# Kernel tuning notes

Measured on AMD Instinct MI355X. Metric: run time of the kernel, lower is better.

## Reference

```python
import jax, jax.numpy as jnp
import numpy as np

B, LQ, LD, H, C = 128, 32, 512, 768, 128


def setup_inputs() -> dict:
    key = jax.random.key(0)
    ks = jax.random.split(key, 8)
    return {
        "query_hidden": jax.random.normal(ks[0], (B, LQ, H), dtype=jnp.float32),
        "doc_hidden": jax.random.normal(ks[1], (B, LD, H), dtype=jnp.float32),
        "query_mask": jax.random.randint(ks[2], (B, LQ), 0, 2, dtype=jnp.int32),
        "doc_mask": jax.random.randint(ks[3], (B, LD), 0, 2, dtype=jnp.int32),
        "W_comp": jax.random.normal(ks[4], (H, C), dtype=jnp.float32) * (1.0 / np.sqrt(H)),
        "b_comp": jax.random.normal(ks[5], (C,), dtype=jnp.float32) * 0.02,
        "w_stop": jax.random.normal(ks[6], (C, 1), dtype=jnp.float32) * (1.0 / np.sqrt(C)),
        "b_stop": jnp.ones((1,), dtype=jnp.float32),  # nn.init.constant_(bias, 1)
        "score_merger": jnp.zeros((1,), dtype=jnp.float32),
    }


def reference(query_hidden, doc_hidden, query_mask, doc_mask,
              W_comp, b_comp, w_stop, b_stop, score_merger):
    qm = query_mask.astype(bool)  # [B, LQ]
    dm = doc_mask.astype(bool)    # [B, LD]

    # encode_shared: CLS vec is the UNcompressed hidden state at position 0
    q_cls = query_hidden[:, 0, :]  # [B, H]
    d_cls = doc_hidden[:, 0, :]    # [B, H]

    # compressor (Linear H->C)
    q_vecs = jnp.einsum('blh,hc->blc', query_hidden, W_comp) + b_comp  # [B, LQ, C]
    d_tok = jnp.einsum('blh,hc->blc', doc_hidden, W_comp) + b_comp     # [B, LD, C]

    # encode_query: zero masked query tokens
    q_vecs = q_vecs * qm[..., None]

    # encode_doc: stopword reducer (relu of Linear C->1), then importance + mask
    importance = jax.nn.relu(jnp.einsum('blc,co->blo', d_tok, w_stop) + b_stop)  # [B, LD, 1]
    d_vecs = d_tok * importance * dm[..., None]

    # CLS score: dot product of (uncompressed) CLS vectors
    cls_score = jnp.sum(q_cls * d_cls, axis=-1)  # [B]

    # term score: MaxSim over doc tokens, masked sum over query tokens
    scores = jnp.einsum('bqc,bkc->bqk', q_vecs, d_vecs)      # [B, LQ, LD]
    scores = jnp.where(dm[:, None, :], scores, -1000.0)
    term = jnp.max(scores, axis=-1)                          # [B, LQ]
    term_score = jnp.sum(jnp.where(qm, term, 0.0), axis=-1)  # [B]

    w = jax.nn.sigmoid(score_merger[0])
    cls_score = cls_score * w
    term_score = term_score * (1.0 - w)
    score = cls_score + term_score
    return (score, cls_score, term_score)
```

## Files before the change

kernel.cpp:

```cpp
#include <hip/hip_runtime.h>
#include <hip/hip_bf16.h>

#define Bb 128
#define LQ 32
#define LD 512
#define Hh 768
#define Cc 128

typedef short bf16x8 __attribute__((ext_vector_type(8)));
typedef float f32x4 __attribute__((ext_vector_type(4)));

__device__ __forceinline__ short f2bf(float f) {
  union { float f; unsigned u; } v;
  v.f = f;
  unsigned u = v.u + (0x7FFFu + ((v.u >> 16) & 1u));
  return (short)(u >> 16);
}

__global__ __launch_bounds__(256) void k_wt(const float* __restrict__ W,
                                            short* __restrict__ Wt) {
  int idx = blockIdx.x * 256 + threadIdx.x;
  int h = idx >> 7;
  int c = idx & 127;
  Wt[c * Hh + h] = f2bf(W[idx]);
}

template <int IS_DOC>
__global__ __launch_bounds__(256) void k_proj(
    const float* __restrict__ X, const short* __restrict__ Wt,
    const float* __restrict__ bcomp, const int* __restrict__ mask,
    const float* __restrict__ wstop, const float* __restrict__ bstop,
    float* __restrict__ Y) {
  const int tid = threadIdx.x;
  const int wave = tid >> 6;
  const int lane = tid & 63;
  const int quad = lane >> 4;
  const int lm = lane & 15;
  const long row0 = (long)blockIdx.x * 128 + wave * 32;

  const float* pa0 = X + (row0 + lm) * Hh + quad * 8;
  const float* pa1 = pa0 + 16 * Hh;
  const short* pbb = Wt + lm * Hh + quad * 8;

  f32x4 acc[2][8];
#pragma unroll
  for (int i = 0; i < 2; ++i)
#pragma unroll
    for (int j = 0; j < 8; ++j) acc[i][j] = (f32x4){0.f, 0.f, 0.f, 0.f};

  for (int kk = 0; kk < Hh; kk += 32) {
    float4 a0l = *(const float4*)(pa0 + kk);
    float4 a0h = *(const float4*)(pa0 + kk + 4);
    float4 a1l = *(const float4*)(pa1 + kk);
    float4 a1h = *(const float4*)(pa1 + kk + 4);
    bf16x8 fb[8];
#pragma unroll
    for (int j = 0; j < 8; ++j)
      fb[j] = *(const bf16x8*)(pbb + j * 16 * Hh + kk);
    bf16x8 fa0, fa1;
    fa0[0] = f2bf(a0l.x); fa0[1] = f2bf(a0l.y);
    fa0[2] = f2bf(a0l.z); fa0[3] = f2bf(a0l.w);
    fa0[4] = f2bf(a0h.x); fa0[5] = f2bf(a0h.y);
    fa0[6] = f2bf(a0h.z); fa0[7] = f2bf(a0h.w);
    fa1[0] = f2bf(a1l.x); fa1[1] = f2bf(a1l.y);
    fa1[2] = f2bf(a1l.z); fa1[3] = f2bf(a1l.w);
    fa1[4] = f2bf(a1h.x); fa1[5] = f2bf(a1h.y);
    fa1[6] = f2bf(a1h.z); fa1[7] = f2bf(a1h.w);
#pragma unroll
    for (int j = 0; j < 8; ++j) {
      acc[0][j] = __builtin_amdgcn_mfma_f32_16x16x32_bf16(fa0, fb[j], acc[0][j], 0, 0, 0);
      acc[1][j] = __builtin_amdgcn_mfma_f32_16x16x32_bf16(fa1, fb[j], acc[1][j], 0, 0, 0);
    }
  }

  float bc[8], ws[8];
#pragma unroll
  for (int j = 0; j < 8; ++j) bc[j] = bcomp[j * 16 + lm];
  if (IS_DOC) {
#pragma unroll
    for (int j = 0; j < 8; ++j) ws[j] = wstop[j * 16 + lm];
  }
  const float bs = IS_DOC ? bstop[0] : 0.f;

#pragma unroll
  for (int i = 0; i < 2; ++i) {
#pragma unroll
    for (int r = 0; r < 4; ++r) {
      const long row = row0 + i * 16 + quad * 4 + r;
      float v[8];
#pragma unroll
      for (int j = 0; j < 8; ++j) v[j] = acc[i][j][r] + bc[j];
      float scale;
      if (IS_DOC) {
        float p = 0.f;
#pragma unroll
        for (int j = 0; j < 8; ++j) p += v[j] * ws[j];
        p += __shfl_xor(p, 1);
        p += __shfl_xor(p, 2);
        p += __shfl_xor(p, 4);
        p += __shfl_xor(p, 8);
        float imp = fmaxf(p + bs, 0.f);
        scale = imp * (float)mask[row];
      } else {
        scale = (float)mask[row];
      }
      float* yr = Y + row * Cc;
#pragma unroll
      for (int j = 0; j < 8; ++j) yr[j * 16 + lm] = v[j] * scale;
    }
  }
}

__global__ __launch_bounds__(256) void k_scores(
    const float* __restrict__ Qv, const float* __restrict__ Dv,
    const int* __restrict__ dmask, float* __restrict__ partial) {
  const int chunk = blockIdx.x;
  const int b = blockIdx.y;
  const int tid = threadIdx.x;
  __shared__ float lq[LQ][Cc + 4];
  __shared__ float ldv[64][Cc + 4];
  __shared__ float pm[LQ][16];
  __shared__ int dmsk[64];

  {
    const float4* src = (const float4*)(Qv + (size_t)b * LQ * Cc);
    for (int i = tid; i < LQ * Cc / 4; i += 256) {
      float4 v = src[i];
      int q = i >> 5;
      int c = (i & 31) << 2;
      *(float4*)&lq[q][c] = v;
    }
  }
  const int k0 = chunk * 64;
  {
    const float4* src = (const float4*)(Dv + ((size_t)b * LD + k0) * Cc);
    for (int i = tid; i < 64 * Cc / 4; i += 256) {
      float4 v = src[i];
      int k = i >> 5;
      int c = (i & 31) << 2;
      *(float4*)&ldv[k][c] = v;
    }
  }
  if (tid < 64) dmsk[tid] = dmask[(size_t)b * LD + k0 + tid];
  __syncthreads();

  const int qt = tid & 15;
  const int kt = tid >> 4;
  const int kbase = kt * 4;
  float a[2][4];
#pragma unroll
  for (int qi = 0; qi < 2; ++qi)
#pragma unroll
    for (int ki = 0; ki < 4; ++ki) a[qi][ki] = 0.f;

  for (int c = 0; c < Cc; c += 4) {
    float4 q0 = *(float4*)&lq[qt][c];
    float4 q1 = *(float4*)&lq[qt + 16][c];
    float4 d0 = *(float4*)&ldv[kbase + 0][c];
    float4 d1 = *(float4*)&ldv[kbase + 1][c];
    float4 d2 = *(float4*)&ldv[kbase + 2][c];
    float4 d3 = *(float4*)&ldv[kbase + 3][c];
    a[0][0] += q0.x * d0.x + q0.y * d0.y + q0.z * d0.z + q0.w * d0.w;
    a[0][1] += q0.x * d1.x + q0.y * d1.y + q0.z * d1.z + q0.w * d1.w;
    a[0][2] += q0.x * d2.x + q0.y * d2.y + q0.z * d2.z + q0.w * d2.w;
    a[0][3] += q0.x * d3.x + q0.y * d3.y + q0.z * d3.z + q0.w * d3.w;
    a[1][0] += q1.x * d0.x + q1.y * d0.y + q1.z * d0.z + q1.w * d0.w;
    a[1][1] += q1.x * d1.x + q1.y * d1.y + q1.z * d1.z + q1.w * d1.w;
    a[1][2] += q1.x * d2.x + q1.y * d2.y + q1.z * d2.z + q1.w * d2.w;
    a[1][3] += q1.x * d3.x + q1.y * d3.y + q1.z * d3.z + q1.w * d3.w;
  }
  float m0 = -1000.f, m1 = -1000.f;
#pragma unroll
  for (int ki = 0; ki < 4; ++ki) {
    if (dmsk[kbase + ki]) {
      m0 = fmaxf(m0, a[0][ki]);
      m1 = fmaxf(m1, a[1][ki]);
    }
  }
  pm[qt][kt] = m0;
  pm[qt + 16][kt] = m1;
  __syncthreads();
  if (tid < LQ) {
    float mx = pm[tid][0];
#pragma unroll
    for (int t = 1; t < 16; ++t) mx = fmaxf(mx, pm[tid][t]);
    partial[((size_t)b * LQ + tid) * 8 + chunk] = mx;
  }
}

__global__ __launch_bounds__(256) void k_final(
    const float* __restrict__ qh, const float* __restrict__ dh,
    const int* __restrict__ qmask, const float* __restrict__ partial,
    const float* __restrict__ merger, float* __restrict__ out) {
  const int b = blockIdx.x;
  const int tid = threadIdx.x;
  __shared__ float red[256];
  __shared__ float clss;
  const float* qc = qh + (size_t)b * LQ * Hh;
  const float* dc = dh + (size_t)b * LD * Hh;
  float s = 0.f;
  for (int h = tid; h < Hh; h += 256) s += qc[h] * dc[h];
  red[tid] = s;
  __syncthreads();
  for (int off = 128; off > 0; off >>= 1) {
    if (tid < off) red[tid] += red[tid + off];
    __syncthreads();
  }
  if (tid == 0) clss = red[0];
  __syncthreads();
  float t = 0.f;
  if (tid < LQ) {
    const float* pp = partial + ((size_t)b * LQ + tid) * 8;
    float mx = pp[0];
#pragma unroll
    for (int c = 1; c < 8; ++c) mx = fmaxf(mx, pp[c]);
    if (qmask[b * LQ + tid]) t = mx;
  }
  red[tid] = t;
  __syncthreads();
  for (int off = 128; off > 0; off >>= 1) {
    if (tid < off) red[tid] += red[tid + off];
    __syncthreads();
  }
  if (tid == 0) {
    float w = 1.f / (1.f + expf(-merger[0]));
    float cs = clss * w;
    float ts = red[0] * (1.f - w);
    out[b] = cs + ts;
    out[Bb + b] = cs;
    out[2 * Bb + b] = ts;
  }
}

extern "C" void kernel_launch(void* const* d_in, const int* in_sizes, int n_in,
                              void* d_out, int out_size, void* d_ws, size_t ws_size,
                              hipStream_t stream) {
  const float* qh  = (const float*)d_in[0];
  const float* dh  = (const float*)d_in[1];
  const int*   qm  = (const int*)d_in[2];
  const int*   dm  = (const int*)d_in[3];
  const float* W   = (const float*)d_in[4];
  const float* bc  = (const float*)d_in[5];
  const float* wst = (const float*)d_in[6];
  const float* bst = (const float*)d_in[7];
  const float* mrg = (const float*)d_in[8];
  float* out = (float*)d_out;

  char* ws = (char*)d_ws;
  short* Wt  = (short*)ws;
  float* qv  = (float*)(ws + 196608);
  float* dv  = (float*)(ws + 196608 + 2097152);
  float* prt = (float*)(ws + 196608 + 2097152 + 33554432);

  k_wt<<<(Hh * Cc) / 256, 256, 0, stream>>>(W, Wt);
  k_proj<0><<<(Bb * LQ) / 128, 256, 0, stream>>>(qh, Wt, bc, qm, nullptr, nullptr, qv);
  k_proj<1><<<(Bb * LD) / 128, 256, 0, stream>>>(dh, Wt, bc, dm, wst, bst, dv);
  k_scores<<<dim3(8, Bb), 256, 0, stream>>>(qv, dv, dm, prt);
  k_final<<<Bb, 256, 0, stream>>>(qh, dh, qm, prt, mrg, out);
}
```

Measured before the change: 398.3 us.

## Merge query and doc projections into one launch with smaller tiles and prefetch

Replaces the two templated projection kernels with a single launch that covers both doc and query rows, dispatching on block index. Each wave now handles 16 rows instead of 32, doubling the block count to improve occupancy and CU coverage. The A operand is software-prefetched one 64-wide K step ahead to hide global load latency. The cost is that each W tile is reused across fewer rows, so more W traffic per row, and the prefetch adds registers and a redundant wraparound load on the last iteration.

```diff
diff --git a/kernel.cpp b/kernel.cpp
--- a/kernel.cpp
+++ b/kernel.cpp
@@ -7,6 +7,9 @@
 #define Hh 768
 #define Cc 128
 
+#define QBLOCKS ((Bb * LQ) / 64)
+#define DBLOCKS ((Bb * LD) / 64)
+
 typedef short bf16x8 __attribute__((ext_vector_type(8)));
 typedef float f32x4 __attribute__((ext_vector_type(4)));
 
@@ -15,6 +18,11 @@
   v.f = f;
   unsigned u = v.u + (0x7FFFu + ((v.u >> 16) & 1u));
   return (short)(u >> 16);
+}
+
+__device__ __forceinline__ void pack8(bf16x8& d, const float4& lo, const float4& hi) {
+  d[0] = f2bf(lo.x); d[1] = f2bf(lo.y); d[2] = f2bf(lo.z); d[3] = f2bf(lo.w);
+  d[4] = f2bf(hi.x); d[5] = f2bf(hi.y); d[6] = f2bf(hi.z); d[7] = f2bf(hi.w);
 }
 
 __global__ __launch_bounds__(256) void k_wt(const float* __restrict__ W,
@@ -25,89 +33,100 @@
   Wt[c * Hh + h] = f2bf(W[idx]);
 }
 
-template <int IS_DOC>
-__global__ __launch_bounds__(256) void k_proj(
-    const float* __restrict__ X, const short* __restrict__ Wt,
-    const float* __restrict__ bcomp, const int* __restrict__ mask,
+__global__ __launch_bounds__(256) void k_proj_all(
+    const float* __restrict__ qh, const float* __restrict__ dh,
+    const short* __restrict__ Wt, const float* __restrict__ bcomp,
+    const int* __restrict__ qmask, const int* __restrict__ dmask,
     const float* __restrict__ wstop, const float* __restrict__ bstop,
-    float* __restrict__ Y) {
+    float* __restrict__ qv, float* __restrict__ dv) {
   const int tid = threadIdx.x;
   const int wave = tid >> 6;
   const int lane = tid & 63;
   const int quad = lane >> 4;
   const int lm = lane & 15;
-  const long row0 = (long)blockIdx.x * 128 + wave * 32;
-
-  const float* pa0 = X + (row0 + lm) * Hh + quad * 8;
-  const float* pa1 = pa0 + 16 * Hh;
-  const short* pbb = Wt + lm * Hh + quad * 8;
-
-  f32x4 acc[2][8];
-#pragma unroll
-  for (int i = 0; i < 2; ++i)
-#pragma unroll
-    for (int j = 0; j < 8; ++j) acc[i][j] = (f32x4){0.f, 0.f, 0.f, 0.f};
-
-  for (int kk = 0; kk < Hh; kk += 32) {
-    float4 a0l = *(const float4*)(pa0 + kk);
-    float4 a0h = *(const float4*)(pa0 + kk + 4);
-    float4 a1l = *(const float4*)(pa1 + kk);
-    float4 a1h = *(const float4*)(pa1 + kk + 4);
-    bf16x8 fb[8];
-#pragma unroll
-    for (int j = 0; j < 8; ++j)
-      fb[j] = *(const bf16x8*)(pbb + j * 16 * Hh + kk);
-    bf16x8 fa0, fa1;
-    fa0[0] = f2bf(a0l.x); fa0[1] = f2bf(a0l.y);
-    fa0[2] = f2bf(a0l.z); fa0[3] = f2bf(a0l.w);
-    fa0[4] = f2bf(a0h.x); fa0[5] = f2bf(a0h.y);
-    fa0[6] = f2bf(a0h.z); fa0[7] = f2bf(a0h.w);
-    fa1[0] = f2bf(a1l.x); fa1[1] = f2bf(a1l.y);
-    fa1[2] = f2bf(a1l.z); fa1[3] = f2bf(a1l.w);
-    fa1[4] = f2bf(a1h.x); fa1[5] = f2bf(a1h.y);
-    fa1[6] = f2bf(a1h.z); fa1[7] = f2bf(a1h.w);
+
+  const int blk = blockIdx.x;
+  const bool is_doc = blk < DBLOCKS;
+  const float* X;
+  float* Y;
+  const int* mask;
+  long row0;
+  if (is_doc) {
+    X = dh; Y = dv; mask = dmask;
+    row0 = (long)blk * 64 + wave * 16;
+  } else {
+    X = qh; Y = qv; mask = qmask;
+    row0 = (long)(blk - DBLOCKS) * 64 + wave * 16;
+  }
+
+  const float* pa = X + (row0 + lm) * (long)Hh + quad * 8;
+  const short* pb = Wt + lm * Hh + quad * 8;
+
+  f32x4 acc[8];
+#pragma unroll
+  for (int j = 0; j < 8; ++j) acc[j] = (f32x4){0.f, 0.f, 0.f, 0.f};
+
+  float4 c0 = *(const float4*)(pa);
+  float4 c1 = *(const float4*)(pa + 4);
+  float4 c2 = *(const float4*)(pa + 32);
+  float4 c3 = *(const float4*)(pa + 36);
+
+  for (int kk = 0; kk < Hh; kk += 64) {
+    int kn = kk + 64;
+    if (kn >= Hh) kn = 0;
+    float4 n0 = *(const float4*)(pa + kn);
+    float4 n1 = *(const float4*)(pa + kn + 4);
+    float4 n2 = *(const float4*)(pa + kn + 32);
+    float4 n3 = *(const float4*)(pa + kn + 36);
+
+    bf16x8 fa;
+    pack8(fa, c0, c1);
 #pragma unroll
     for (int j = 0; j < 8; ++j) {
-      acc[0][j] = __builtin_amdgcn_mfma_f32_16x16x32_bf16(fa0, fb[j], acc[0][j], 0, 0, 0);
-      acc[1][j] = __builtin_amdgcn_mfma_f32_16x16x32_bf16(fa1, fb[j], acc[1][j], 0, 0, 0);
-    }
-  }
-
-  float bc[8], ws[8];
+      bf16x8 fb = *(const bf16x8*)(pb + j * 16 * Hh + kk);
+      acc[j] = __builtin_amdgcn_mfma_f32_16x16x32_bf16(fa, fb, acc[j], 0, 0, 0);
+    }
+    pack8(fa, c2, c3);
+#pragma unroll
+    for (int j = 0; j < 8; ++j) {
+      bf16x8 fb = *(const bf16x8*)(pb + j * 16 * Hh + kk + 32);
+      acc[j] = __builtin_amdgcn_mfma_f32_16x16x32_bf16(fa, fb, acc[j], 0, 0, 0);
+    }
+    c0 = n0; c1 = n1; c2 = n2; c3 = n3;
+  }
+
+  float bc[8], wsv[8];
 #pragma unroll
   for (int j = 0; j < 8; ++j) bc[j] = bcomp[j * 16 + lm];
-  if (IS_DOC) {
-#pragma unroll
-    for (int j = 0; j < 8; ++j) ws[j] = wstop[j * 16 + lm];
-  }
-  const float bs = IS_DOC ? bstop[0] : 0.f;
-
-#pragma unroll
-  for (int i = 0; i < 2; ++i) {
-#pragma unroll
-    for (int r = 0; r < 4; ++r) {
-      const long row = row0 + i * 16 + quad * 4 + r;
-      float v[8];
-#pragma unroll
-      for (int j = 0; j < 8; ++j) v[j] = acc[i][j][r] + bc[j];
-      float scale;
-      if (IS_DOC) {
-        float p = 0.f;
-#pragma unroll
-        for (int j = 0; j < 8; ++j) p += v[j] * ws[j];
-        p += __shfl_xor(p, 1);
-        p += __shfl_xor(p, 2);
-        p += __shfl_xor(p, 4);
-        p += __shfl_xor(p, 8);
-        float imp = fmaxf(p + bs, 0.f);
-        scale = imp * (float)mask[row];
-      } else {
-        scale = (float)mask[row];
-      }
-      float* yr = Y + row * Cc;
-#pragma unroll
-      for (int j = 0; j < 8; ++j) yr[j * 16 + lm] = v[j] * scale;
-    }
+  if (is_doc) {
+#pragma unroll
+    for (int j = 0; j < 8; ++j) wsv[j] = wstop[j * 16 + lm];
+  }
+  const float bs = is_doc ? bstop[0] : 0.f;
+
+#pragma unroll
+  for (int r = 0; r < 4; ++r) {
+    const long row = row0 + quad * 4 + r;
+    float v[8];
+#pragma unroll
+    for (int j = 0; j < 8; ++j) v[j] = acc[j][r] + bc[j];
+    float scale;
+    if (is_doc) {
+      float p = 0.f;
+#pragma unroll
+      for (int j = 0; j < 8; ++j) p += v[j] * wsv[j];
+      p += __shfl_xor(p, 1);
+      p += __shfl_xor(p, 2);
+      p += __shfl_xor(p, 4);
+      p += __shfl_xor(p, 8);
+      float imp = fmaxf(p + bs, 0.f);
+      scale = imp * (float)mask[row];
+    } else {
+      scale = (float)mask[row];
+    }
+    float* yr = Y + row * Cc;
+#pragma unroll
+    for (int j = 0; j < 8; ++j) yr[j * 16 + lm] = v[j] * scale;
   }
 }
 
@@ -253,8 +272,8 @@
   float* prt = (float*)(ws + 196608 + 2097152 + 33554432);
 
   k_wt<<<(Hh * Cc) / 256, 256, 0, stream>>>(W, Wt);
-  k_proj<0><<<(Bb * LQ) / 128, 256, 0, stream>>>(qh, Wt, bc, qm, nullptr, nullptr, qv);
-  k_proj<1><<<(Bb * LD) / 128, 256, 0, stream>>>(dh, Wt, bc, dm, wst, bst, dv);
+  k_proj_all<<<DBLOCKS + QBLOCKS, 256, 0, stream>>>(qh, dh, Wt, bc, qm, dm,
+                                                    wst, bst, qv, dv);
   k_scores<<<dim3(8, Bb), 256, 0, stream>>>(qv, dv, dm, prt);
   k_final<<<Bb, 256, 0, stream>>>(qh, dh, qm, prt, mrg, out);
 }
```

New measurement: 395.8 us. About the same (-0.6%).
